# Kernel tuning notes

Hardware: AMD Instinct MI355X
Metric: run time of the kernel (lower is better)

The kernel has to match this reference:

```python
import jax, jax.numpy as jnp
import numpy as np

# Coefficients of the 16 differentiable logic gates expressed over the basis
# [1, a, b, a*b]. Row i corresponds to gate i in the standard difflogic order:
# 0:0, 1:a&b, 2:a&~b, 3:a, 4:~a&b, 5:b, 6:xor, 7:or, 8:nor, 9:xnor,
# 10:~b, 11:b=>a, 12:~a, 13:a=>b, 14:nand, 15:1
GATE_COEFFS = np.array([
    [0, 0, 0, 0],
    [0, 0, 0, 1],
    [0, 1, 0, -1],
    [0, 1, 0, 0],
    [0, 0, 1, -1],
    [0, 0, 1, 0],
    [0, 1, 1, -2],
    [0, 1, 1, -1],
    [1, -1, -1, 1],
    [1, -1, -1, 2],
    [1, 0, -1, 0],
    [1, 0, -1, 1],
    [1, -1, 0, 0],
    [1, -1, 0, 1],
    [1, 0, 0, -1],
    [1, 0, 0, 0],
], dtype=np.float32)

IN_DIM = 8192
OUT_DIM = 8192
BATCH = 8192
TAU = 1.0


def setup_inputs() -> dict:
    key = jax.random.key(0)
    k1, k2, k3, k4 = jax.random.split(key, 4)
    x = jax.random.uniform(k1, (BATCH, IN_DIM), dtype=jnp.float32)
    weight = jax.random.normal(k2, (OUT_DIM, 16), dtype=jnp.float32)
    idx_a = jax.random.randint(k3, (OUT_DIM,), 0, IN_DIM, dtype=jnp.int64 if jax.config.jax_enable_x64 else jnp.int32)
    idx_b = jax.random.randint(k4, (OUT_DIM,), 0, IN_DIM, dtype=jnp.int64 if jax.config.jax_enable_x64 else jnp.int32)
    return {"x": x, "weight": weight, "idx_a": idx_a, "idx_b": idx_b}


def reference(x, weight, idx_a, idx_b):
    # Gather the two inputs of each neuron: [B, out_dim]
    a = x[:, idx_a]
    b = x[:, idx_b]
    # Soft gate mixture: softmax over 16 gates per neuron (training, 'soft')
    w = jax.nn.softmax(weight / TAU, axis=-1)  # [out_dim, 16]
    # Since every gate is affine in {1, a, b, ab}, collapse the 16-gate
    # weighted sum into per-neuron coefficients: c = w @ G  -> [out_dim, 4]
    c = w @ jnp.asarray(GATE_COEFFS)
    out = c[:, 0] + c[:, 1] * a + c[:, 2] * b + c[:, 3] * (a * b)
    return out
```

## Files before the change

### kernel.cpp

```cpp
#include <hip/hip_runtime.h>
#include <math.h>

#define IN_DIM  8192
#define OUT_DIM 8192
#define BATCH   8192
#define ROWS    16
#define T       1024

__device__ __constant__ float GC0[16] = {0,0,0,0, 0,0,0,0, 1,1,1,1, 1,1,1,1};
__device__ __constant__ float GC1[16] = {0,0,1,1, 0,0,1,1, -1,-1,0,0, -1,-1,0,0};
__device__ __constant__ float GC2[16] = {0,0,0,0, 1,1,1,1, -1,-1,-1,-1, 0,0,0,0};
__device__ __constant__ float GC3[16] = {0,1,-1,0, -1,0,-2,-1, 1,2,0,1, 0,1,-1,0};

__global__ __launch_bounds__(256) void compute_c_kernel(
    const float* __restrict__ weight, float4* __restrict__ c)
{
    int row = blockIdx.x * 256 + threadIdx.x;
    if (row >= OUT_DIM) return;
    const float* wr = weight + (size_t)row * 16;
    float v[16];
    float m = -1e30f;
#pragma unroll
    for (int i = 0; i < 16; ++i) { v[i] = wr[i]; m = fmaxf(m, v[i]); }
    float s = 0.f;
#pragma unroll
    for (int i = 0; i < 16; ++i) { v[i] = __expf(v[i] - m); s += v[i]; }
    float inv = 1.0f / s;
    float c0 = 0.f, c1 = 0.f, c2 = 0.f, c3 = 0.f;
#pragma unroll
    for (int i = 0; i < 16; ++i) {
        c0 = fmaf(v[i], GC0[i], c0);
        c1 = fmaf(v[i], GC1[i], c1);
        c2 = fmaf(v[i], GC2[i], c2);
        c3 = fmaf(v[i], GC3[i], c3);
    }
    c[row] = make_float4(c0 * inv, c1 * inv, c2 * inv, c3 * inv);
}

__global__ __launch_bounds__(T, 4) void gate_main_kernel(
    const float* __restrict__ x,
    const float4* __restrict__ c,
    const int4* __restrict__ ia4,
    const int4* __restrict__ ib4,
    float4* __restrict__ out)
{
    __shared__ float buf[2][IN_DIM];
    const int tid = threadIdx.x;
    const size_t r0 = (size_t)blockIdx.x * ROWS;

    const int q0 = tid, q1 = tid + T;
    const int4 iaA = ia4[q0], ibA = ib4[q0];
    const int4 iaB = ia4[q1], ibB = ib4[q1];
    const float4 cA0 = c[4*q0+0], cA1 = c[4*q0+1], cA2 = c[4*q0+2], cA3 = c[4*q0+3];
    const float4 cB0 = c[4*q1+0], cB1 = c[4*q1+1], cB2 = c[4*q1+2], cB3 = c[4*q1+3];

    {
        const float4* src4 = (const float4*)(x + r0 * IN_DIM);
        float4* dst4 = (float4*)buf[0];
        dst4[tid]     = src4[tid];
        dst4[tid + T] = src4[tid + T];
    }
    __syncthreads();

    int cur = 0;
    for (int r = 0; r < ROWS; ++r) {
        float4 p0 = make_float4(0,0,0,0), p1 = make_float4(0,0,0,0);
        if (r + 1 < ROWS) {
            const float4* src4 = (const float4*)(x + (r0 + r + 1) * IN_DIM);
            p0 = src4[tid];
            p1 = src4[tid + T];
        }

        const float* xr = buf[cur];
        float4* orow = out + (r0 + r) * (OUT_DIM / 4);
        {
            float a0 = xr[iaA.x], b0 = xr[ibA.x];
            float a1 = xr[iaA.y], b1 = xr[ibA.y];
            float a2 = xr[iaA.z], b2 = xr[ibA.z];
            float a3 = xr[iaA.w], b3 = xr[ibA.w];
            float4 o;
            o.x = fmaf(a0, fmaf(b0, cA0.w, cA0.y), fmaf(b0, cA0.z, cA0.x));
            o.y = fmaf(a1, fmaf(b1, cA1.w, cA1.y), fmaf(b1, cA1.z, cA1.x));
            o.z = fmaf(a2, fmaf(b2, cA2.w, cA2.y), fmaf(b2, cA2.z, cA2.x));
            o.w = fmaf(a3, fmaf(b3, cA3.w, cA3.y), fmaf(b3, cA3.z, cA3.x));
            orow[q0] = o;
        }
        {
            float a0 = xr[iaB.x], b0 = xr[ibB.x];
            float a1 = xr[iaB.y], b1 = xr[ibB.y];
            float a2 = xr[iaB.z], b2 = xr[ibB.z];
            float a3 = xr[iaB.w], b3 = xr[ibB.w];
            float4 o;
            o.x = fmaf(a0, fmaf(b0, cB0.w, cB0.y), fmaf(b0, cB0.z, cB0.x));
            o.y = fmaf(a1, fmaf(b1, cB1.w, cB1.y), fmaf(b1, cB1.z, cB1.x));
            o.z = fmaf(a2, fmaf(b2, cB2.w, cB2.y), fmaf(b2, cB2.z, cB2.x));
            o.w = fmaf(a3, fmaf(b3, cB3.w, cB3.y), fmaf(b3, cB3.z, cB3.x));
            orow[q1] = o;
        }

        if (r + 1 < ROWS) {
            float4* dst4 = (float4*)buf[cur ^ 1];
            dst4[tid]     = p0;
            dst4[tid + T] = p1;
        }
        __syncthreads();
        cur ^= 1;
    }
}

extern "C" void kernel_launch(void* const* d_in, const int* in_sizes, int n_in,
                              void* d_out, int out_size, void* d_ws, size_t ws_size,
                              hipStream_t stream) {
    const float* x      = (const float*)d_in[0];
    const float* weight = (const float*)d_in[1];
    const int*   idx_a  = (const int*)d_in[2];
    const int*   idx_b  = (const int*)d_in[3];
    float* out = (float*)d_out;

    float4* c = (float4*)d_ws;

    compute_c_kernel<<<OUT_DIM / 256, 256, 0, stream>>>(weight, c);
    gate_main_kernel<<<BATCH / ROWS, T, 0, stream>>>(
        x, c, (const int4*)idx_a, (const int4*)idx_b, (float4*)out);
}
```

Before: 445.9 us.

## Prefetch x rows directly into LDS via global_load_lds and double rows per block

Replaces the register-staged prefetch of the next x row (global load to VGPR, then LDS store) with direct global-to-LDS DMA loads, using explicit vmcnt waits and raw barriers. It also doubles the rows handled per block, which halves the number of blocks and amortizes the per-block load of indices and coefficients. The aim is to cut VGPR pressure and LDS store instructions on the staging path. The risks are that the hand-written waitcnt(2) sequencing is fragile because output stores also count toward vmcnt, and that fewer blocks lowers occupancy and parallelism.

```diff
diff --git a/kernel.cpp b/kernel.cpp
--- a/kernel.cpp
+++ b/kernel.cpp
@@ -4,8 +4,12 @@
 #define IN_DIM  8192
 #define OUT_DIM 8192
 #define BATCH   8192
-#define ROWS    16
+#define ROWS    32
 #define T       1024
+
+#define GLOAD_LDS16(g, l) __builtin_amdgcn_global_load_lds( \
+    (const __attribute__((address_space(1))) void*)(g),     \
+    (__attribute__((address_space(3))) void*)(l), 16, 0, 0)
 
 __device__ __constant__ float GC0[16] = {0,0,0,0, 0,0,0,0, 1,1,1,1, 1,1,1,1};
 __device__ __constant__ float GC1[16] = {0,0,1,1, 0,0,1,1, -1,-1,0,0, -1,-1,0,0};
@@ -45,7 +49,8 @@
     float4* __restrict__ out)
 {
     __shared__ float buf[2][IN_DIM];
-    const int tid = threadIdx.x;
+    const int tid  = threadIdx.x;
+    const int wave = tid >> 6;
     const size_t r0 = (size_t)blockIdx.x * ROWS;
 
     const int q0 = tid, q1 = tid + T;
@@ -55,21 +60,23 @@
     const float4 cB0 = c[4*q1+0], cB1 = c[4*q1+1], cB2 = c[4*q1+2], cB3 = c[4*q1+3];
 
     {
-        const float4* src4 = (const float4*)(x + r0 * IN_DIM);
-        float4* dst4 = (float4*)buf[0];
-        dst4[tid]     = src4[tid];
-        dst4[tid + T] = src4[tid + T];
+        const float* src = x + r0 * IN_DIM;
+        GLOAD_LDS16(src + (tid << 2),        &buf[0][wave << 8]);
+        GLOAD_LDS16(src + 4096 + (tid << 2), &buf[0][4096 + (wave << 8)]);
     }
-    __syncthreads();
+    asm volatile("s_waitcnt vmcnt(0)" ::: "memory");
+    __builtin_amdgcn_s_barrier();
 
-    int cur = 0;
     for (int r = 0; r < ROWS; ++r) {
-        float4 p0 = make_float4(0,0,0,0), p1 = make_float4(0,0,0,0);
+        const int cur = r & 1;
+
         if (r + 1 < ROWS) {
-            const float4* src4 = (const float4*)(x + (r0 + r + 1) * IN_DIM);
-            p0 = src4[tid];
-            p1 = src4[tid + T];
+            const float* src = x + (r0 + r + 1) * IN_DIM;
+            float* bn = buf[cur ^ 1];
+            GLOAD_LDS16(src + (tid << 2),        bn + (wave << 8));
+            GLOAD_LDS16(src + 4096 + (tid << 2), bn + 4096 + (wave << 8));
         }
+        asm volatile("" ::: "memory");
 
         const float* xr = buf[cur];
         float4* orow = out + (r0 + r) * (OUT_DIM / 4);
@@ -99,12 +106,9 @@
         }
 
         if (r + 1 < ROWS) {
-            float4* dst4 = (float4*)buf[cur ^ 1];
-            dst4[tid]     = p0;
-            dst4[tid + T] = p1;
+            asm volatile("s_waitcnt vmcnt(2)" ::: "memory");
+            __builtin_amdgcn_s_barrier();
         }
-        __syncthreads();
-        cur ^= 1;
     }
 }
 
```

After: 446.3 us. Within noise of the previous version (+0.1%).
